# Kernel tuning notes

Hardware: AMD Instinct MI355X
Metric: run time of the kernel (lower is better)

## Reference

```python
import jax, jax.numpy as jnp
import numpy as np

EPS = 0.05
ITERS = 3


def setup_inputs() -> dict:
    key = jax.random.key(0)
    ks = jax.random.split(key, 20)
    B, C, H, W, TD = 2, 256, 64, 64, 512
    s = 0.02
    inp = {
        "img_feat": jax.random.normal(ks[0], (B, C, H, W), jnp.float32),
        "txt_feat": jax.random.normal(ks[1], (B, TD), jnp.float32),
        "density_map": jax.random.uniform(ks[2], (B, 1, H, W), jnp.float32),
        # text_proj
        "Wt": jax.random.normal(ks[3], (C, TD), jnp.float32) * s,
        "bt": jnp.zeros((C,), jnp.float32),
        # gamma_fc / beta_fc
        "Wg": jax.random.normal(ks[4], (C, C), jnp.float32) * s,
        "bg": jnp.zeros((C,), jnp.float32),
        "Wb": jax.random.normal(ks[5], (C, C), jnp.float32) * s,
        "bb": jnp.zeros((C,), jnp.float32),
        # out_proj 1x1 conv as [O, I]
        "Wo": jax.random.normal(ks[6], (C, C), jnp.float32) * s,
        "bo": jnp.zeros((C,), jnp.float32),
        # heatmap head: conv3x3 -> BN -> ReLU -> conv1x1
        "Wc1": jax.random.normal(ks[7], (C // 2, C, 3, 3), jnp.float32) * s,
        "bc1": jnp.zeros((C // 2,), jnp.float32),
        "bn_g": jnp.ones((C // 2,), jnp.float32),
        "bn_b": jnp.zeros((C // 2,), jnp.float32),
        "Wc2": jax.random.normal(ks[8], (2, C // 2), jnp.float32) * s,
        "bc2": jnp.zeros((2,), jnp.float32),
    }
    return inp


def reference(img_feat, txt_feat, density_map, Wt, bt, Wg, bg, Wb, bb,
              Wo, bo, Wc1, bc1, bn_g, bn_b, Wc2, bc2):
    B, C, H, W = img_feat.shape
    N = H * W

    # FiLM-style modulation from text
    txt_emb = txt_feat @ Wt.T + bt                         # [B, C]
    gamma = (txt_emb @ Wg.T + bg)[:, :, None, None]        # [B, C, 1, 1]
    beta = (txt_emb @ Wb.T + bb)[:, :, None, None]
    mod = img_feat * (1.0 + gamma) + beta                  # [B, C, H, W]

    source_feat = mod.reshape(B, C, N).transpose(0, 2, 1)  # [B, N, C]

    # marginals
    target = jax.nn.relu(density_map.reshape(B, N)) + 1e-6
    q = target / jnp.sum(target, axis=1, keepdims=True)    # [B, N]
    p = jnp.full((B, N), 1.0 / N, img_feat.dtype)

    # cosine-similarity cost and Gibbs kernel
    src_n = source_feat / jnp.maximum(
        jnp.linalg.norm(source_feat, axis=2, keepdims=True), 1e-12)
    sim = jnp.einsum('bnc,bmc->bnm', src_n, src_n)         # [B, N, N]
    K = jnp.exp(-(1.0 - sim) / EPS)

    # Sinkhorn iterations (fixed count)
    u = jnp.ones_like(p)
    v = jnp.ones_like(q)
    for _ in range(ITERS):
        v = q / (jnp.einsum('bnm,bn->bm', K, u) + 1e-8)
        u = p / (jnp.einsum('bnm,bm->bn', K, v) + 1e-8)

    T = u[:, :, None] * K * v[:, None, :]                  # transport plan
    fused = jnp.einsum('bnm,bnc->bmc', T, source_feat)     # T^T @ source
    fused = fused.transpose(0, 2, 1).reshape(B, C, H, W)

    out_feat = img_feat + jnp.einsum('oc,bchw->bohw', Wo, fused) + bo[None, :, None, None]

    # heatmap head
    h = jax.lax.conv_general_dilated(
        out_feat, Wc1, window_strides=(1, 1), padding='SAME',
        dimension_numbers=('NCHW', 'OIHW', 'NCHW')) + bc1[None, :, None, None]
    m = jnp.mean(h, axis=(0, 2, 3), keepdims=True)
    var = jnp.var(h, axis=(0, 2, 3), keepdims=True)
    h = (h - m) * jax.lax.rsqrt(var + 1e-5)
    h = jax.nn.relu(h * bn_g[None, :, None, None] + bn_b[None, :, None, None])
    heatmap = jnp.einsum('oc,bchw->bohw', Wc2, h) + bc2[None, :, None, None]

    return out_feat, heatmap
```

## Files before the change

### kernel.cpp

```cpp
#include <hip/hip_runtime.h>
#include <stdint.h>

#define B_   2
#define C_   256
#define N_   4096
#define TD_  512
#define OC_  128
#define PW_  66
#define PA_  4356

typedef float  f32x4  __attribute__((ext_vector_type(4)));
typedef short  bf16x8 __attribute__((ext_vector_type(8)));
typedef unsigned short u16;
typedef unsigned char  u8;

__device__ __forceinline__ u16 f2bf(float x){
  union { float f; uint32_t u; } v; v.f = x;
  uint32_t r = v.u + 0x7fffu + ((v.u >> 16) & 1u);
  return (u16)(r >> 16);
}
__device__ __forceinline__ uint32_t f2e5m2(float x){
  x = fminf(fmaxf(x, -57344.f), 57344.f);
  union { _Float16 h; u16 u; } c; c.h = (_Float16)x;
  uint32_t hb = c.u;
  return ((hb + 0x7fu + ((hb >> 8) & 1u)) >> 8) & 0xffu;
}
__device__ __forceinline__ float e5m2f(uint32_t byte){
  union { u16 u; _Float16 h; } c; c.u = (u16)(byte << 8);
  return (float)c.h;
}

__device__ __forceinline__ void gld_lds16(const void* g, void* l){
  __builtin_amdgcn_global_load_lds(
      (const __attribute__((address_space(1))) unsigned int*)g,
      (__attribute__((address_space(3))) unsigned int*)l,
      16, 0, 0);
}

__global__ __launch_bounds__(1024) void k_prep(
    const float* __restrict__ txt, const float* __restrict__ Wt, const float* __restrict__ bt,
    const float* __restrict__ Wg, const float* __restrict__ bg,
    const float* __restrict__ Wb, const float* __restrict__ bb,
    const float* __restrict__ dens, const float* __restrict__ Wo, const float* __restrict__ Wc1,
    float* __restrict__ gamma, float* __restrict__ beta,
    float* __restrict__ q, float* __restrict__ u,
    u16* __restrict__ Wo_bf, u16* __restrict__ Wc1r, u16* __restrict__ P){
  int bid = blockIdx.x;
  int t = threadIdx.x;
  if (bid < 2){
    int b = bid;
    __shared__ float ts[TD_];
    __shared__ float te[C_];
    if (t < TD_) ts[t] = txt[b*TD_ + t];
    __syncthreads();
    {
      int c = t >> 2, p = t & 3;
      const float4* w4 = (const float4*)(Wt + (size_t)c*TD_ + p*128);
      const float4* t4 = (const float4*)(ts + p*128);
      float a = 0.f;
      #pragma unroll 8
      for (int j = 0; j < 32; j++){
        float4 wv = w4[j], tv = t4[j];
        a += wv.x*tv.x + wv.y*tv.y + wv.z*tv.z + wv.w*tv.w;
      }
      a += __shfl_xor(a, 1);
      a += __shfl_xor(a, 2);
      if (p == 0) te[c] = a + bt[c];
    }
    __syncthreads();
    {
      int c = t >> 2, qb = (t >> 1) & 1, p = t & 1;
      const float* W = qb ? Wb : Wg;
      const float4* w4 = (const float4*)(W + (size_t)c*C_ + p*128);
      const float4* t4 = (const float4*)(te + p*128);
      float a = 0.f;
      #pragma unroll 8
      for (int j = 0; j < 32; j++){
        float4 wv = w4[j], tv = t4[j];
        a += wv.x*tv.x + wv.y*tv.y + wv.z*tv.z + wv.w*tv.w;
      }
      a += __shfl_xor(a, 1);
      if (p == 0){
        if (qb) beta[b*C_ + c]  = a + bb[c];
        else    gamma[b*C_ + c] = a + bg[c];
      }
    }
  } else if (bid < 4){
    int b = bid - 2;
    __shared__ float red[1024];
    float s = 0.f;
    for (int i = t; i < N_; i += 1024){ float v = fmaxf(dens[b*N_ + i], 0.f) + 1e-6f; s += v; }
    red[t] = s; __syncthreads();
    for (int o = 512; o; o >>= 1){ if (t < o) red[t] += red[t + o]; __syncthreads(); }
    float invs = 1.f / red[0];
    for (int i = t; i < N_; i += 1024){
      float v = fmaxf(dens[b*N_ + i], 0.f) + 1e-6f;
      q[b*N_ + i] = v*invs;
      u[b*N_ + i] = 1.f;
    }
  } else if (bid < 292){
    int i = (bid - 4)*1024 + t;
    if (i < C_*C_) Wo_bf[i] = f2bf(Wo[i]);
    if (i < 9*OC_*C_){
      int s = i / (OC_*C_); int rem = i - s*(OC_*C_);
      int oc = rem >> 8; int ic = rem & 255;
      Wc1r[i] = f2bf(Wc1[((size_t)(oc*C_ + ic))*9 + s]);
    }
  } else {
    int g = (bid - 292)*1024 + t;
    if (g < 16640){
      int px_i = g >> 5, seg = g & 31;
      int b = (px_i >= 260) ? 1 : 0;
      int i = px_i - b*260;
      int row, col;
      if (i < 66)      { row = 0;  col = i; }
      else if (i < 132){ row = 65; col = i - 66; }
      else { int i2 = i - 132; row = 1 + (i2 >> 1); col = (i2 & 1) ? 65 : 0; }
      uint4 z; z.x = 0; z.y = 0; z.z = 0; z.w = 0;
      *(uint4*)((char*)P + ((size_t)(b*PA_ + row*PW_ + col))*512 + seg*16) = z;
    }
  }
}

__global__ __launch_bounds__(256) void k_build(
    const float* __restrict__ img, const float* __restrict__ gamma, const float* __restrict__ beta,
    u16* __restrict__ Sn){
  int b = blockIdx.y; int n0 = blockIdx.x*64;
  __shared__ float tile[C_][65];
  __shared__ float pss[4][64];
  __shared__ float inv[64];
  int t = threadIdx.x;
  int x = t & 63, cb = t >> 6;
  float ss = 0.f;
  for (int k = 0; k < 64; k++){
    int c = cb*64 + k;
    float v = img[((size_t)(b*C_ + c))*N_ + n0 + x];
    v = v*(1.f + gamma[b*C_ + c]) + beta[b*C_ + c];
    tile[c][x] = v;
    ss += v*v;
  }
  pss[cb][x] = ss;
  __syncthreads();
  if (t < 64){
    float s = pss[0][t] + pss[1][t] + pss[2][t] + pss[3][t];
    float nrm = sqrtf(s);
    inv[t] = 1.f / fmaxf(nrm, 1e-12f);
  }
  __syncthreads();
  for (int i = 0; i < 64; i++){
    int idx = i*256 + t;
    int c = idx & 255, nl = idx >> 8;
    Sn[((size_t)(b*N_ + n0 + nl))*C_ + c] = f2bf(tile[c][nl]*inv[nl]);
  }
}

__global__ __launch_bounds__(256) void k_simK(const u16* __restrict__ Sn, u8* __restrict__ K8,
                                              u8* __restrict__ flags){
  int idx = blockIdx.x;
  int b = blockIdx.z;
  int nt = (int)((sqrtf(8.f*idx + 1.f) - 1.f)*0.5f);
  while ((nt+1)*(nt+2)/2 <= idx) nt++;
  while (nt*(nt+1)/2 > idx) nt--;
  int mt = idx - nt*(nt+1)/2;
  __shared__ char smem[32768];
  __shared__ int fred[4];
  int t = threadIdx.x; int w = t >> 6; int l = t & 63;
  int wm = w >> 1, wn = w & 1;
  f32x4 acc[4][4] = {};
  const char* Ab = (const char*)(Sn + ((size_t)(b*N_ + mt*128))*C_);
  const char* Bb = (const char*)(Sn + ((size_t)(b*N_ + nt*128))*C_);
  for (int step = 0; step < 4; step++){
    __syncthreads();
    for (int r = 0; r < 4; r++){
      int off = r*4096 + t*16;
      int row = off >> 7;
      int col = (off & 127) ^ ((row & 7) << 4);
      gld_lds16(Ab + (size_t)row*512 + step*128 + col, smem + off);
      gld_lds16(Bb + (size_t)row*512 + step*128 + col, smem + 16384 + off);
    }
    __syncthreads();
    for (int kk = 0; kk < 2; kk++){
      bf16x8 af[4], bfv[4];
      for (int i = 0; i < 4; i++){
        int ra = wm*64 + i*16 + (l & 15);
        af[i]  = *(const bf16x8*)(smem + ((ra*128 + kk*64 + (l>>4)*16) ^ ((ra & 7) << 4)));
        int rb = wn*64 + i*16 + (l & 15);
        bfv[i] = *(const bf16x8*)(smem + 16384 + ((rb*128 + kk*64 + (l>>4)*16) ^ ((rb & 7) << 4)));
      }
      for (int i = 0; i < 4; i++)
        for (int j = 0; j < 4; j++)
          acc[i][j] = __builtin_amdgcn_mfma_f32_16x16x32_bf16(af[i], bfv[j], acc[i][j], 0, 0, 0);
    }
  }
  float tmax = -1.f;
  for (int i = 0; i < 4; i++)
    for (int j = 0; j < 4; j++){
      f32x4 a = acc[i][j];
      tmax = fmaxf(tmax, fmaxf(fmaxf(a[0], a[1]), fmaxf(a[2], a[3])));
    }
  int nz = __any(tmax > 0.40f) ? 1 : 0;
  if (l == 0) fred[w] = nz;
  __syncthreads();
  int F = fred[0] | fred[1] | fred[2] | fred[3];
  if (t == 0){
    flags[b*1024 + nt*32 + mt] = (u8)F;
    if (mt != nt) flags[b*1024 + mt*32 + nt] = (u8)F;
  }
  size_t gb  = ((size_t)(b*N_ + nt*128))*N_ + mt*128;
  size_t gb2 = ((size_t)(b*N_ + mt*128))*N_ + nt*128;
  if (!F){
    uint4 z; z.x = 0; z.y = 0; z.z = 0; z.w = 0;
    for (int p = 0; p < 4; p++){
      int id2 = p*256 + t;
      int R = id2 >> 3, sl = id2 & 7;
      *(uint4*)(K8 + gb + (size_t)R*N_ + sl*16) = z;
      if (mt != nt) *(uint4*)(K8 + gb2 + (size_t)R*N_ + sl*16) = z;
    }
    return;
  }
  u8* tile = (u8*)smem;
  uint32_t wds[4][4];
  for (int i = 0; i < 4; i++)
    for (int j = 0; j < 4; j++){
      int R  = wn*64 + j*16 + (l & 15);
      int Cc = wm*64 + i*16 + ((l >> 4) << 2);
      uint32_t wd =  f2e5m2(__expf((acc[i][j][0] - 1.f)*20.f))
                  | (f2e5m2(__expf((acc[i][j][1] - 1.f)*20.f)) << 8)
                  | (f2e5m2(__expf((acc[i][j][2] - 1.f)*20.f)) << 16)
                  | (f2e5m2(__expf((acc[i][j][3] - 1.f)*20.f)) << 24);
      wds[i][j] = wd;
      *(uint32_t*)(tile + ((R*128 + Cc) ^ ((R & 7) << 4))) = wd;
    }
  __syncthreads();
  for (int p = 0; p < 4; p++){
    int id2 = p*256 + t;
    int R = id2 >> 3, sl = id2 & 7;
    uint4 vv = *(const uint4*)(tile + ((R*128 + sl*16) ^ ((R & 7) << 4)));
    *(uint4*)(K8 + gb + (size_t)R*N_ + sl*16) = vv;
  }
  if (mt != nt){
    __syncthreads();
    for (int i = 0; i < 4; i++)
      for (int j = 0; j < 4; j++){
        int m0 = wm*64 + i*16 + ((l >> 4) << 2);
        int n  = wn*64 + j*16 + (l & 15);
        uint32_t wd = wds[i][j];
        for (int r = 0; r < 4; r++){
          int R = m0 + r;
          tile[(R*128 + n) ^ ((R & 7) << 4)] = (u8)(wd >> (8*r));
        }
      }
    __syncthreads();
    for (int p = 0; p < 4; p++){
      int id2 = p*256 + t;
      int R = id2 >> 3, sl = id2 & 7;
      uint4 vv = *(const uint4*)(tile + ((R*128 + sl*16) ^ ((R & 7) << 4)));
      *(uint4*)(K8 + gb2 + (size_t)R*N_ + sl*16) = vv;
    }
  }
}

__global__ __launch_bounds__(256) void k_sink(
    const u8* __restrict__ K8, const u8* __restrict__ flags,
    const float* __restrict__ q,
    const float* __restrict__ img, const float* __restrict__ gamma,
    const float* __restrict__ beta,
    float* __restrict__ u, float* __restrict__ v, u8* __restrict__ uS8){
  int r = blockIdx.x, b = blockIdx.y;
  int t = threadIdx.x;
  __shared__ uint32_t mask[32];
  __shared__ uint32_t comp_s;
  __shared__ u8 tl[32];
  __shared__ int scnt;
  __shared__ float xb[4096];
  __shared__ float yb[4096];
  if (t < 32){
    const u8* fr = flags + b*1024 + t*32;
    uint32_t m = 0;
    for (int j = 0; j < 32; j++) m |= (uint32_t)(fr[j] != 0) << j;
    mask[t] = m;
  }
  __syncthreads();
  if (t == 0){
    uint32_t comp = 1u << r;
    for (int it = 0; it < 32; it++){
      uint32_t nc = comp;
      for (int i = 0; i < 32; i++) if ((comp >> i) & 1u) nc |= mask[i];
      if (nc == comp) break;
      comp = nc;
    }
    comp_s = comp;
    int c = 0;
    for (int i = 0; i < 32; i++) if ((comp >> i) & 1u) tl[c++] = (u8)i;
    scnt = c;
  }
  __syncthreads();
  uint32_t comp = comp_s;
  if (comp & ((1u << r) - 1u)) return;
  int s = scnt;
  int R = s*128;
  for (int i = t; i < R; i += 256) xb[i] = 1.f;
  __syncthreads();
  for (int it = 0; it < 6; it++){
    int use_q = !(it & 1);
    for (int ri = t; ri < R; ri += 256){
      int gm = tl[ri >> 7]*128 + (ri & 127);
      const u8* kp = K8 + ((size_t)(b*N_ + gm))*N_;
      float ssum = 0.f;
      for (int ci = 0; ci < s; ci++){
        const u8* kt = kp + tl[ci]*128;
        const float* xp = xb + ci*128;
        for (int kk = 0; kk < 16; kk++){
          uint2 kv = *(const uint2*)(kt + kk*8);
          const float* x8 = xp + kk*8;
          ssum += e5m2f( kv.x        & 0xff)*x8[0] + e5m2f((kv.x >>  8) & 0xff)*x8[1]
                + e5m2f((kv.x >> 16) & 0xff)*x8[2] + e5m2f( kv.x >> 24        )*x8[3];
          ssum += e5m2f( kv.y        & 0xff)*x8[4] + e5m2f((kv.y >>  8) & 0xff)*x8[5]
                + e5m2f((kv.y >> 16) & 0xff)*x8[6] + e5m2f( kv.y >> 24        )*x8[7];
        }
      }
      float marg = use_q ? q[b*N_ + gm] : 2.44140625e-4f;
      yb[ri] = marg / (ssum + 1e-8f);
    }
    __syncthreads();
    if (it == 4)
      for (int i = t; i < R; i += 256) v[b*N_ + tl[i >> 7]*128 + (i & 127)] = yb[i];
    if (it == 5)
      for (int i = t; i < R; i += 256) u[b*N_ + tl[i >> 7]*128 + (i & 127)] = yb[i];
    for (int i = t; i < R; i += 256) xb[i] = yb[i];
    __syncthreads();
  }
  int qpc = R >> 2;
  int quads = C_ * qpc;
  for (int qd = t; qd < quads; qd += 256){
    int c  = qd / qpc;
    int nq = qd - c*qpc;
    int ri = nq*4;
    int n = tl[ri >> 7]*128 + (ri & 127);
    size_t bc = (size_t)(b*C_ + c);
    float gm = 1.f + gamma[bc];
    float bt = beta[bc];
    float4 vi = *(const float4*)(img + bc*N_ + n);
    uint32_t o =  f2e5m2((vi.x*gm + bt)*xb[ri+0])
               | (f2e5m2((vi.y*gm + bt)*xb[ri+1]) << 8)
               | (f2e5m2((vi.z*gm + bt)*xb[ri+2]) << 16)
               | (f2e5m2((vi.w*gm + bt)*xb[ri+3]) << 24);
    *(uint32_t*)(uS8 + bc*N_ + n) = o;
  }
}

__global__ __launch_bounds__(256) void k_fused(
    const u8* __restrict__ K8, const u8* __restrict__ uS8, const u8* __restrict__ flags,
    const float* __restrict__ vvec, u16* __restrict__ fused){
  int ct = blockIdx.x;
  int mt = blockIdx.y, b = blockIdx.z;
  __shared__ char smem[32768];
  int t = threadIdx.x, w = t >> 6, l = t & 63;
  int wc = w >> 1, wm = w & 1;
  f32x4 acc[4][4] = {};
  const u8* Ab = uS8 + ((size_t)(b*C_ + ct*128))*N_;
  const u8* Bb = K8  + ((size_t)(b*N_ + mt*128))*N_;
  const u8* fr = flags + b*1024 + mt*32;
  for (int step = 0; step < 32; step++){
    if (!fr[step]) continue;
    __syncthreads();
    for (int r = 0; r < 4; r++){
      int off = r*4096 + t*16;
      int row = off >> 7;
      int col = (off & 127) ^ ((row & 7) << 4);
      gld_lds16(Ab + (size_t)row*N_ + step*128 + col, smem + off);
      gld_lds16(Bb + (size_t)row*N_ + step*128 + col, smem + 16384 + off);
    }
    __syncthreads();
    for (int kk = 0; kk < 4; kk++){
      long av[4], bv[4];
      for (int i = 0; i < 4; i++){
        int ra = wc*64 + i*16 + (l & 15);
        av[i] = *(const long*)(smem + ((ra*128 + kk*32 + (l>>4)*8) ^ ((ra & 7) << 4)));
        int rb = wm*64 + i*16 + (l & 15);
        bv[i] = *(const long*)(smem + 16384 + ((rb*128 + kk*32 + (l>>4)*8) ^ ((rb & 7) << 4)));
      }
      for (int i = 0; i < 4; i++)
        for (int j = 0; j < 4; j++)
          acc[i][j] = __builtin_amdgcn_mfma_f32_16x16x32_bf8_bf8(av[i], bv[j], acc[i][j], 0, 0, 0);
    }
  }
  for (int j = 0; j < 4; j++){
    int m = mt*128 + wm*64 + j*16 + (l & 15);
    float vm = vvec[b*N_ + m];
    for (int i = 0; i < 4; i++){
      int c0 = ct*128 + wc*64 + i*16 + ((l >> 4) << 2);
      ushort4 o;
      o.x = f2bf(acc[i][j][0]*vm);
      o.y = f2bf(acc[i][j][1]*vm);
      o.z = f2bf(acc[i][j][2]*vm);
      o.w = f2bf(acc[i][j][3]*vm);
      *(ushort4*)(fused + ((size_t)(b*N_ + m))*C_ + c0) = o;
    }
  }
}

__global__ __launch_bounds__(256) void k_outproj(
    const u16* __restrict__ fused, const u16* __restrict__ Wo_bf,
    const float* __restrict__ img, const float* __restrict__ bo,
    float* __restrict__ out, u16* __restrict__ P){
  int nt = blockIdx.x, ot = blockIdx.y, b = blockIdx.z;
  int t = threadIdx.x, w = t >> 6, l = t & 63;
  int wm = w >> 1, wn = w & 1;
  __shared__ u16 tile[128][72];
  f32x4 acc[4][2] = {};
  for (int kc = 0; kc < 8; kc++){
    bf16x8 af[4], bfv[2];
    for (int i = 0; i < 4; i++){
      int n = nt*128 + wm*64 + i*16 + (l & 15);
      af[i] = *(const bf16x8*)(fused + ((size_t)(b*N_ + n))*C_ + kc*32 + (l >> 4)*8);
    }
    for (int j = 0; j < 2; j++){
      int o = ot*64 + wn*32 + j*16 + (l & 15);
      bfv[j] = *(const bf16x8*)(Wo_bf + (size_t)o*C_ + kc*32 + (l >> 4)*8);
    }
    for (int i = 0; i < 4; i++)
      for (int j = 0; j < 2; j++)
        acc[i][j] = __builtin_amdgcn_mfma_f32_16x16x32_bf16(af[i], bfv[j], acc[i][j], 0, 0, 0);
  }
  for (int i = 0; i < 4; i++)
    for (int j = 0; j < 2; j++){
      int ol = wn*32 + j*16 + (l & 15);
      int o = ot*64 + ol;
      int nl = wm*64 + i*16 + ((l >> 4) << 2);
      int n = nt*128 + nl;
      size_t a = ((size_t)(b*C_ + o))*N_ + n;
      float4 iv = *(const float4*)(img + a);
      float bov = bo[o];
      float4 r;
      r.x = iv.x + acc[i][j][0] + bov;
      r.y = iv.y + acc[i][j][1] + bov;
      r.z = iv.z + acc[i][j][2] + bov;
      r.w = iv.w + acc[i][j][3] + bov;
      *(float4*)(out + a) = r;
      tile[nl+0][ol] = f2bf(r.x);
      tile[nl+1][ol] = f2bf(r.y);
      tile[nl+2][ol] = f2bf(r.z);
      tile[nl+3][ol] = f2bf(r.w);
    }
  __syncthreads();
  for (int p = 0; p < 4; p++){
    int idx = p*256 + t;
    int row = idx >> 3, seg = idx & 7;
    int n = nt*128 + row;
    int y = n >> 6, x = n & 63;
    uint4 vv = *(const uint4*)(&tile[row][seg*8]);
    *(uint4*)(P + ((size_t)(b*PA_ + (y+1)*PW_ + (x+1)))*C_ + ot*64 + seg*8) = vv;
  }
}

__global__ __launch_bounds__(256) void k_conv(
    const u16* __restrict__ P, const u16* __restrict__ Wc1r, float* __restrict__ convP){
  int pt = blockIdx.x;
  int sp = blockIdx.y;
  int b  = blockIdx.z;
  int dy = sp - 1;
  __shared__ char smem[32768];
  int t = threadIdx.x, w = t >> 6, l = t & 63;
  int wm = w >> 1, wn = w & 1;
  f32x4 acc[4][4] = {};
  int y0 = pt*2;
  size_t prow[4], wrow[4];
  int colsw[4];
  #pragma unroll
  for (int rr = 0; rr < 4; rr++){
    int off = rr*4096 + t*16;
    int row = off >> 7;
    int col = (off & 127) ^ ((row & 7) << 4);
    colsw[rr] = col;
    int gy = row >> 6, gx = row & 63;
    prow[rr] = ((size_t)(b*PA_ + (y0 + gy + dy + 1)*PW_ + gx + 1))*512;
    wrow[rr] = ((size_t)(sp*3*128 + row))*512;
  }
  const char* Pb = (const char*)P;
  const char* Wb = (const char*)Wc1r;
  for (int step = 0; step < 12; step++){
    int dxi = step >> 2, c64 = step & 3;
    __syncthreads();
    #pragma unroll
    for (int rr = 0; rr < 4; rr++){
      int off = rr*4096 + t*16;
      gld_lds16(Wb + wrow[rr] + (size_t)dxi*65536 + c64*128 + colsw[rr], smem + off);
      gld_lds16(Pb + prow[rr] + (dxi-1)*512 + c64*128 + colsw[rr], smem + 16384 + off);
    }
    __syncthreads();
    for (int kk = 0; kk < 2; kk++){
      bf16x8 af[4], bv[4];
      for (int i = 0; i < 4; i++){
        int ra = wm*64 + i*16 + (l & 15);
        af[i] = *(const bf16x8*)(smem + ((ra*128 + kk*64 + (l>>4)*16) ^ ((ra & 7) << 4)));
        int rb = wn*64 + i*16 + (l & 15);
        bv[i] = *(const bf16x8*)(smem + 16384 + ((rb*128 + kk*64 + (l>>4)*16) ^ ((rb & 7) << 4)));
      }
      for (int i = 0; i < 4; i++)
        for (int j = 0; j < 4; j++)
          acc[i][j] = __builtin_amdgcn_mfma_f32_16x16x32_bf16(af[i], bv[j], acc[i][j], 0, 0, 0);
    }
  }
  float* pp = convP + (((size_t)(sp*2 + b))*N_ + (size_t)pt*128)*OC_;
  for (int i = 0; i < 4; i++)
    for (int j = 0; j < 4; j++){
      int pxl = wn*64 + j*16 + (l & 15);
      int ocl = wm*64 + i*16 + ((l >> 4) << 2);
      float4 r; r.x = acc[i][j][0]; r.y = acc[i][j][1]; r.z = acc[i][j][2]; r.w = acc[i][j][3];
      *(float4*)(pp + (size_t)pxl*OC_ + ocl) = r;
    }
}

__global__ __launch_bounds__(256) void k_stats(
    const float* __restrict__ convP, const float* __restrict__ bc1,
    float* __restrict__ h, float* __restrict__ pSum, float* __restrict__ pSsq){
  int blk = blockIdx.x;
  int t = threadIdx.x; int c = t & 127, half = t >> 7;
  __shared__ float s1[256], s2[256];
  float bias = bc1[c];
  float a = 0.f, b2 = 0.f;
  int R0 = blk*128 + half*64;
  for (int r = 0; r < 64; r++){
    size_t base = (size_t)(R0 + r)*OC_ + c;
    float v = convP[base] + convP[base + (size_t)8192*OC_] + convP[base + (size_t)16384*OC_] + bias;
    h[base] = v;
    a += v; b2 += v*v;
  }
  s1[t] = a; s2[t] = b2;
  __syncthreads();
  if (t < 128){
    pSum[blk*128 + c] = s1[t] + s1[t + 128];
    pSsq[blk*128 + c] = s2[t] + s2[t + 128];
  }
}

__global__ __launch_bounds__(256) void k_head(
    const float* __restrict__ h, const float* __restrict__ pSum, const float* __restrict__ pSsq,
    const float* __restrict__ bn_g, const float* __restrict__ bn_b,
    const float* __restrict__ Wc2, const float* __restrict__ bc2, float* __restrict__ hm){
  __shared__ float sc[128], sh[128], w0[128], w1[128];
  __shared__ float rs[256], rss[256];
  int t = threadIdx.x;
  {
    int c = t & 127, half = t >> 7;
    float s = 0.f, ss = 0.f;
    for (int k = half*32; k < half*32 + 32; k++){
      s += pSum[k*128 + c]; ss += pSsq[k*128 + c];
    }
    rs[t] = s; rss[t] = ss;
  }
  __syncthreads();
  if (t < 128){
    float s = rs[t] + rs[t+128], ss = rss[t] + rss[t+128];
    float m = s*(1.f/8192.f);
    float var = ss*(1.f/8192.f) - m*m;
    float scv = bn_g[t]*rsqrtf(var + 1e-5f);
    sc[t] = scv; sh[t] = bn_b[t] - m*scv;
    w0[t] = Wc2[t]; w1[t] = Wc2[128 + t];
  }
  __syncthreads();
  int n = blockIdx.x*256 + t;
  const float* hp = h + (size_t)n*OC_;
  float a0 = bc2[0], a1 = bc2[1];
  for (int c4 = 0; c4 < 32; c4++){
    float4 hv = *(const float4*)(hp + c4*4);
    int c = c4*4;
    float r;
    r = fmaxf(hv.x*sc[c]   + sh[c],   0.f); a0 += w0[c]*r;   a1 += w1[c]*r;
    r = fmaxf(hv.y*sc[c+1] + sh[c+1], 0.f); a0 += w0[c+1]*r; a1 += w1[c+1]*r;
    r = fmaxf(hv.z*sc[c+2] + sh[c+2], 0.f); a0 += w0[c+2]*r; a1 += w1[c+2]*r;
    r = fmaxf(hv.w*sc[c+3] + sh[c+3], 0.f); a0 += w0[c+3]*r; a1 += w1[c+3]*r;
  }
  int b = n >> 12, p = n & 4095;
  hm[((size_t)(b*2 + 0))*N_ + p] = a0;
  hm[((size_t)(b*2 + 1))*N_ + p] = a1;
}

extern "C" void kernel_launch(void* const* d_in, const int* in_sizes, int n_in,
                              void* d_out, int out_size, void* d_ws, size_t ws_size,
                              hipStream_t stream){
  const float* img  = (const float*)d_in[0];
  const float* txt  = (const float*)d_in[1];
  const float* dens = (const float*)d_in[2];
  const float* Wt   = (const float*)d_in[3];
  const float* bt   = (const float*)d_in[4];
  const float* Wg   = (const float*)d_in[5];
  const float* bg   = (const float*)d_in[6];
  const float* Wb   = (const float*)d_in[7];
  const float* bb   = (const float*)d_in[8];
  const float* Wo   = (const float*)d_in[9];
  const float* bo   = (const float*)d_in[10];
  const float* Wc1  = (const float*)d_in[11];
  const float* bc1  = (const float*)d_in[12];
  const float* bng  = (const float*)d_in[13];
  const float* bnb  = (const float*)d_in[14];
  const float* Wc2  = (const float*)d_in[15];
  const float* bc2  = (const float*)d_in[16];

  char* ws = (char*)d_ws;
  u8*       K8     = (u8*)      (ws + 0);
  u16*      Sn     = (u16*)     (ws + 33554432);
  u8*       uS8    = (u8*)      (ws + 37748736);
  u16*      fused  = (u16*)     (ws + 56623104);
  u16*      P      = (u16*)     (ws + 60817408);
  float*    hbuf   = (float*)   (ws + 65277952);
  float*    convP  = (float*)   (ws + 69472256);
  float*    gamma  = (float*)   (ws + 82055168);
  float*    beta   = (float*)   (ws + 82057216);
  float*    q      = (float*)   (ws + 82059264);
  float*    u      = (float*)   (ws + 82092032);
  float*    v      = (float*)   (ws + 82124800);
  u16*      Wo_bf  = (u16*)     (ws + 82157568);
  u16*      Wc1r   = (u16*)     (ws + 82288640);
  float*    pSum   = (float*)   (ws + 82878464);
  float*    pSsq   = (float*)   (ws + 82911232);
  u8*       flags  = (u8*)      (ws + 82944000);

  float* outp = (float*)d_out;
  float* hm   = outp + 2*C_*N_;

  k_prep  <<<309, 1024, 0, stream>>>(txt, Wt, bt, Wg, bg, Wb, bb, dens, Wo, Wc1,
                                     gamma, beta, q, u, Wo_bf, Wc1r, P);
  k_build <<<dim3(64,2), 256, 0, stream>>>(img, gamma, beta, Sn);
  k_simK  <<<dim3(528,1,2), 256, 0, stream>>>(Sn, K8, flags);
  k_sink  <<<dim3(32,2), 256, 0, stream>>>(K8, flags, q, img, gamma, beta, u, v, uS8);
  k_fused <<<dim3(2,32,2), 256, 0, stream>>>(K8, uS8, flags, v, fused);
  k_outproj<<<dim3(32,4,2), 256, 0, stream>>>(fused, Wo_bf, img, bo, outp, P);
  k_conv  <<<dim3(32,3,2), 256, 0, stream>>>(P, Wc1r, convP);
  k_stats <<<64, 256, 0, stream>>>(convP, bc1, hbuf, pSum, pSsq);
  k_head  <<<32, 256, 0, stream>>>(hbuf, pSum, pSsq, bng, bnb, Wc2, bc2, hm);
}
```

Before: 142.7 us.

## Skip zero-tile K writes, mask sparse tiles in Sinkhorn, fuse conv with BN stats

k_simK no longer writes zeros for tiles flagged as negligible. k_sink instead skips those tiles using a per-row-tile mask, which avoids both the zero stores and the reads of those bytes. The conv kernel now accumulates all three dy rows in one block instead of splitting them across blocks. It adds the bias and computes the BN partial sums in-kernel, which removes the convP round trip and the separate stats kernel. The risks are that any other consumer of K8 (k_fused) could read stale memory on skipped tiles, and that the conv grid shrinks to 64 blocks, which lowers parallelism.

```diff
diff --git a/kernel.cpp b/kernel.cpp
--- a/kernel.cpp
+++ b/kernel.cpp
@@ -206,18 +206,9 @@
     flags[b*1024 + nt*32 + mt] = (u8)F;
     if (mt != nt) flags[b*1024 + mt*32 + nt] = (u8)F;
   }
+  if (!F) return;
   size_t gb  = ((size_t)(b*N_ + nt*128))*N_ + mt*128;
   size_t gb2 = ((size_t)(b*N_ + mt*128))*N_ + nt*128;
-  if (!F){
-    uint4 z; z.x = 0; z.y = 0; z.z = 0; z.w = 0;
-    for (int p = 0; p < 4; p++){
-      int id2 = p*256 + t;
-      int R = id2 >> 3, sl = id2 & 7;
-      *(uint4*)(K8 + gb + (size_t)R*N_ + sl*16) = z;
-      if (mt != nt) *(uint4*)(K8 + gb2 + (size_t)R*N_ + sl*16) = z;
-    }
-    return;
-  }
   u8* tile = (u8*)smem;
   uint32_t wds[4][4];
   for (int i = 0; i < 4; i++)
@@ -304,10 +295,13 @@
   for (int it = 0; it < 6; it++){
     int use_q = !(it & 1);
     for (int ri = t; ri < R; ri += 256){
-      int gm = tl[ri >> 7]*128 + (ri & 127);
+      int rt = tl[ri >> 7];
+      int gm = rt*128 + (ri & 127);
       const u8* kp = K8 + ((size_t)(b*N_ + gm))*N_;
+      uint32_t rowmask = mask[rt];
       float ssum = 0.f;
       for (int ci = 0; ci < s; ci++){
+        if (!((rowmask >> tl[ci]) & 1u)) continue;
         const u8* kt = kp + tl[ci]*128;
         const float* xp = xb + ci*128;
         for (int kk = 0; kk < 16; kk++){
@@ -455,17 +449,16 @@
 }
 
 __global__ __launch_bounds__(256) void k_conv(
-    const u16* __restrict__ P, const u16* __restrict__ Wc1r, float* __restrict__ convP){
+    const u16* __restrict__ P, const u16* __restrict__ Wc1r, const float* __restrict__ bc1,
+    float* __restrict__ h, float* __restrict__ pSum, float* __restrict__ pSsq){
   int pt = blockIdx.x;
-  int sp = blockIdx.y;
-  int b  = blockIdx.z;
-  int dy = sp - 1;
+  int b  = blockIdx.y;
   __shared__ char smem[32768];
   int t = threadIdx.x, w = t >> 6, l = t & 63;
   int wm = w >> 1, wn = w & 1;
   f32x4 acc[4][4] = {};
   int y0 = pt*2;
-  size_t prow[4], wrow[4];
+  size_t prowB[4], wrowB[4];
   int colsw[4];
   #pragma unroll
   for (int rr = 0; rr < 4; rr++){
@@ -474,19 +467,24 @@
     int col = (off & 127) ^ ((row & 7) << 4);
     colsw[rr] = col;
     int gy = row >> 6, gx = row & 63;
-    prow[rr] = ((size_t)(b*PA_ + (y0 + gy + dy + 1)*PW_ + gx + 1))*512;
-    wrow[rr] = ((size_t)(sp*3*128 + row))*512;
+    prowB[rr] = ((size_t)(b*PA_ + (y0 + gy + 1)*PW_ + gx + 1))*512;
+    wrowB[rr] = (size_t)row*512;
   }
   const char* Pb = (const char*)P;
   const char* Wb = (const char*)Wc1r;
-  for (int step = 0; step < 12; step++){
-    int dxi = step >> 2, c64 = step & 3;
+  for (int step = 0; step < 36; step++){
+    int sp  = step / 12;
+    int rem = step - sp*12;
+    int dxi = rem >> 2, c64 = rem & 3;
+    int s = sp*3 + dxi;
+    long pShift = (long)(sp - 1)*(PW_*512) + (long)(dxi - 1)*512 + c64*128;
+    size_t wShift = (size_t)s*65536 + (size_t)c64*128;
     __syncthreads();
     #pragma unroll
     for (int rr = 0; rr < 4; rr++){
       int off = rr*4096 + t*16;
-      gld_lds16(Wb + wrow[rr] + (size_t)dxi*65536 + c64*128 + colsw[rr], smem + off);
-      gld_lds16(Pb + prow[rr] + (dxi-1)*512 + c64*128 + colsw[rr], smem + 16384 + off);
+      gld_lds16(Wb + wrowB[rr] + wShift + colsw[rr], smem + off);
+      gld_lds16(Pb + (long)prowB[rr] + pShift + colsw[rr], smem + 16384 + off);
     }
     __syncthreads();
     for (int kk = 0; kk < 2; kk++){
@@ -502,36 +500,57 @@
           acc[i][j] = __builtin_amdgcn_mfma_f32_16x16x32_bf16(af[i], bv[j], acc[i][j], 0, 0, 0);
     }
   }
-  float* pp = convP + (((size_t)(sp*2 + b))*N_ + (size_t)pt*128)*OC_;
+  __syncthreads();
+  float* sL = (float*)smem;
+  float* qL = (float*)(smem + 1024);
+  float sv[4][4], qv[4][4];
+  #pragma unroll
   for (int i = 0; i < 4; i++)
+    #pragma unroll
+    for (int e = 0; e < 4; e++){ sv[i][e] = 0.f; qv[i][e] = 0.f; }
+  #pragma unroll
+  for (int i = 0; i < 4; i++){
+    int ocl = wm*64 + i*16 + ((l >> 4) << 2);
+    float4 bc = *(const float4*)(bc1 + ocl);
+    #pragma unroll
     for (int j = 0; j < 4; j++){
       int pxl = wn*64 + j*16 + (l & 15);
+      float4 r;
+      r.x = acc[i][j][0] + bc.x;
+      r.y = acc[i][j][1] + bc.y;
+      r.z = acc[i][j][2] + bc.z;
+      r.w = acc[i][j][3] + bc.w;
+      *(float4*)(h + ((size_t)(b*N_ + pt*128 + pxl))*OC_ + ocl) = r;
+      sv[i][0] += r.x;     sv[i][1] += r.y;     sv[i][2] += r.z;     sv[i][3] += r.w;
+      qv[i][0] += r.x*r.x; qv[i][1] += r.y*r.y; qv[i][2] += r.z*r.z; qv[i][3] += r.w*r.w;
+    }
+  }
+  #pragma unroll
+  for (int o = 1; o < 16; o <<= 1){
+    #pragma unroll
+    for (int i = 0; i < 4; i++)
+      #pragma unroll
+      for (int e = 0; e < 4; e++){
+        sv[i][e] += __shfl_xor(sv[i][e], o);
+        qv[i][e] += __shfl_xor(qv[i][e], o);
+      }
+  }
+  if ((l & 15) == 0){
+    #pragma unroll
+    for (int i = 0; i < 4; i++){
       int ocl = wm*64 + i*16 + ((l >> 4) << 2);
-      float4 r; r.x = acc[i][j][0]; r.y = acc[i][j][1]; r.z = acc[i][j][2]; r.w = acc[i][j][3];
-      *(float4*)(pp + (size_t)pxl*OC_ + ocl) = r;
-    }
-}
-
-__global__ __launch_bounds__(256) void k_stats(
-    const float* __restrict__ convP, const float* __restrict__ bc1,
-    float* __restrict__ h, float* __restrict__ pSum, float* __restrict__ pSsq){
-  int blk = blockIdx.x;
-  int t = threadIdx.x; int c = t & 127, half = t >> 7;
-  __shared__ float s1[256], s2[256];
-  float bias = bc1[c];
-  float a = 0.f, b2 = 0.f;
-  int R0 = blk*128 + half*64;
-  for (int r = 0; r < 64; r++){
-    size_t base = (size_t)(R0 + r)*OC_ + c;
-    float v = convP[base] + convP[base + (size_t)8192*OC_] + convP[base + (size_t)16384*OC_] + bias;
-    h[base] = v;
-    a += v; b2 += v*v;
-  }
-  s1[t] = a; s2[t] = b2;
+      #pragma unroll
+      for (int e = 0; e < 4; e++){
+        sL[wn*128 + ocl + e] = sv[i][e];
+        qL[wn*128 + ocl + e] = qv[i][e];
+      }
+    }
+  }
   __syncthreads();
   if (t < 128){
-    pSum[blk*128 + c] = s1[t] + s1[t + 128];
-    pSsq[blk*128 + c] = s2[t] + s2[t + 128];
+    int blk = b*32 + pt;
+    pSum[blk*128 + t] = sL[t] + sL[128 + t];
+    pSsq[blk*128 + t] = qL[t] + qL[128 + t];
   }
 }
 
@@ -605,7 +624,6 @@
   u16*      fused  = (u16*)     (ws + 56623104);
   u16*      P      = (u16*)     (ws + 60817408);
   float*    hbuf   = (float*)   (ws + 65277952);
-  float*    convP  = (float*)   (ws + 69472256);
   float*    gamma  = (float*)   (ws + 82055168);
   float*    beta   = (float*)   (ws + 82057216);
   float*    q      = (float*)   (ws + 82059264);
@@ -627,7 +645,6 @@
   k_sink  <<<dim3(32,2), 256, 0, stream>>>(K8, flags, q, img, gamma, beta, u, v, uS8);
   k_fused <<<dim3(2,32,2), 256, 0, stream>>>(K8, uS8, flags, v, fused);
   k_outproj<<<dim3(32,4,2), 256, 0, stream>>>(fused, Wo_bf, img, bo, outp, P);
-  k_conv  <<<dim3(32,3,2), 256, 0, stream>>>(P, Wc1r, convP);
-  k_stats <<<64, 256, 0, stream>>>(convP, bc1, hbuf, pSum, pSsq);
+  k_conv  <<<dim3(32,2), 256, 0, stream>>>(P, Wc1r, bc1, hbuf, pSum, pSsq);
   k_head  <<<32, 256, 0, stream>>>(hbuf, pSum, pSsq, bng, bnb, Wc2, bc2, hm);
 }
```

Result: slower. 160.3 us (+12.3%).
